# Kernel optimization log

Hardware: AMD Instinct MI355X
Metric: run time of the kernel (lower is better)

Reference implementation:

```python
import jax, jax.numpy as jnp
import numpy as np

IN_FEATURES = 4096
OUT_FEATURES = 4096
SHARED_ROWS = 256
BATCH = 8192


def setup_inputs() -> dict:
    key = jax.random.key(0)
    k_x, k_w, k_b = jax.random.split(key, 3)
    x = jax.random.normal(k_x, (BATCH, IN_FEATURES), dtype=jnp.float32)
    shared_weights = jax.random.normal(k_w, (SHARED_ROWS, IN_FEATURES), dtype=jnp.float32)
    bias = jax.random.normal(k_b, (OUT_FEATURES,), dtype=jnp.float32)
    return {"x": x, "shared_weights": shared_weights, "bias": bias}


def reference(x, shared_weights, bias):
    # Faithful to torch: weight_matrix = shared_weights.repeat(out//shared, 1)
    reps = OUT_FEATURES // SHARED_ROWS
    weight_matrix = jnp.tile(shared_weights, (reps, 1))  # [out_features, in_features]
    # y = x @ W^T + b  -> [batch, out_features]
    return jnp.matmul(x, weight_matrix.T) + bias
```

## Files before the change

kernel.cpp:

```cpp
#include <hip/hip_runtime.h>
#include <cstdint>
#include <cstddef>

#define M_DIM 8192
#define N_DIM 256
#define K_DIM 4096
#define OUT_F 4096
#define BM 32
#define BK 64
#define NTH 512
#define LDK 72

typedef float    float4_  __attribute__((ext_vector_type(4)));
typedef _Float16 half8    __attribute__((ext_vector_type(8)));
typedef _Float16 half4    __attribute__((ext_vector_type(4)));

__global__ __launch_bounds__(256) void convert_w_kernel(const float* __restrict__ w,
                                                        _Float16* __restrict__ wh) {
  int i = (blockIdx.x * 256 + threadIdx.x) * 8;
  float4_ f0 = *(const float4_*)(w + i);
  float4_ f1 = *(const float4_*)(w + i + 4);
  half8 h;
  h[0] = (_Float16)f0[0]; h[1] = (_Float16)f0[1];
  h[2] = (_Float16)f0[2]; h[3] = (_Float16)f0[3];
  h[4] = (_Float16)f1[0]; h[5] = (_Float16)f1[1];
  h[6] = (_Float16)f1[2]; h[7] = (_Float16)f1[3];
  *(half8*)(wh + i) = h;
}

__device__ __forceinline__ void load_bfrag(half8 b[2][2],
                                           const _Float16* __restrict__ wg0,
                                           const _Float16* __restrict__ wg1,
                                           int kk) {
#pragma unroll
  for (int ks = 0; ks < 2; ++ks) {
    b[ks][0] = *(const half8*)(wg0 + kk + ks * 32);
    b[ks][1] = *(const half8*)(wg1 + kk + ks * 32);
  }
}

__device__ __forceinline__ void stage_a(_Float16 (*As)[LDK], int arow, int acol,
                                        float4_ a) {
  half4 h;
  h[0] = (_Float16)a[0]; h[1] = (_Float16)a[1];
  h[2] = (_Float16)a[2]; h[3] = (_Float16)a[3];
  *(half4*)(&As[arow][acol]) = h;
}

__device__ __forceinline__ void mfma_step(float4_ acc[2][2], const half8 b[2][2],
                                          const _Float16 (*As)[LDK],
                                          int l16, int quad) {
#pragma unroll
  for (int ks = 0; ks < 2; ++ks) {
    const int koff = ks * 32 + quad * 8;
    half8 a0 = *(const half8*)(&As[l16][koff]);
    half8 a1 = *(const half8*)(&As[16 + l16][koff]);
    acc[0][0] = __builtin_amdgcn_mfma_f32_16x16x32_f16(a0, b[ks][0], acc[0][0], 0, 0, 0);
    acc[1][0] = __builtin_amdgcn_mfma_f32_16x16x32_f16(a1, b[ks][0], acc[1][0], 0, 0, 0);
    acc[0][1] = __builtin_amdgcn_mfma_f32_16x16x32_f16(a0, b[ks][1], acc[0][1], 0, 0, 0);
    acc[1][1] = __builtin_amdgcn_mfma_f32_16x16x32_f16(a1, b[ks][1], acc[1][1], 0, 0, 0);
  }
}

__global__ __launch_bounds__(NTH, 2) void fused_kernel(const float* __restrict__ x,
                                                       const _Float16* __restrict__ wh,
                                                       const float* __restrict__ bias,
                                                       float* __restrict__ out) {
  __shared__ __align__(16) _Float16 As[2][BM][LDK];
  __shared__ __align__(16) float Ssh[BM][N_DIM + 4];
  __shared__ __align__(16) float bsh[OUT_F];

  const int tid  = threadIdx.x;
  const int wv   = tid >> 6;
  const int lane = tid & 63;
  const int quad = lane >> 4;
  const int l16  = lane & 15;
  const int n0   = wv * 32;
  const int m0   = blockIdx.x * BM;

  {
    const float4_* b4 = (const float4_*)bias;
    float4_* bs4 = (float4_*)bsh;
    bs4[tid] = b4[tid];
    bs4[NTH + tid] = b4[NTH + tid];
  }

  const int arow = tid >> 4;
  const int acol = (tid & 15) * 4;
  const float* xg = x + (size_t)(m0 + arow) * K_DIM + acol;

  const _Float16* wg0 = wh + (size_t)(n0 + l16) * K_DIM + quad * 8;
  const _Float16* wg1 = wg0 + (size_t)16 * K_DIM;

  float4_ acc[2][2];
  const float4_ fzero = {0.f, 0.f, 0.f, 0.f};
#pragma unroll
  for (int i = 0; i < 2; ++i)
#pragma unroll
    for (int j = 0; j < 2; ++j) acc[i][j] = fzero;

  half8 bA[2][2], bB[2][2];
  float4_ aP0 = __builtin_nontemporal_load((const float4_*)(xg));
  float4_ aP1 = __builtin_nontemporal_load((const float4_*)(xg + BK));
  load_bfrag(bA, wg0, wg1, 0);
  stage_a(As[0], arow, acol, aP0);
  aP0 = __builtin_nontemporal_load((const float4_*)(xg + 2 * BK));
  __syncthreads();

  const int NKT = K_DIM / BK;
  for (int kt = 0; kt < NKT; kt += 2) {
    load_bfrag(bB, wg0, wg1, (kt + 1) * BK);
    stage_a(As[1], arow, acol, aP1);
    if (kt + 3 < NKT)
      aP1 = __builtin_nontemporal_load((const float4_*)(xg + (kt + 3) * BK));
    mfma_step(acc, bA, As[0], l16, quad);
    __syncthreads();

    if (kt + 2 < NKT) {
      load_bfrag(bA, wg0, wg1, (kt + 2) * BK);
      stage_a(As[0], arow, acol, aP0);
      if (kt + 4 < NKT)
        aP0 = __builtin_nontemporal_load((const float4_*)(xg + (kt + 4) * BK));
    }
    mfma_step(acc, bB, As[1], l16, quad);
    __syncthreads();
  }

#pragma unroll
  for (int mf = 0; mf < 2; ++mf)
#pragma unroll
    for (int nf = 0; nf < 2; ++nf)
#pragma unroll
      for (int r = 0; r < 4; ++r)
        Ssh[mf * 16 + quad * 4 + r][n0 + nf * 16 + l16] = acc[mf][nf][r];
  __syncthreads();

  float4_ s[4];
#pragma unroll
  for (int rr = 0; rr < 4; ++rr)
    s[rr] = *(const float4_*)(&Ssh[wv * 4 + rr][lane * 4]);

  float4_* o0 = (float4_*)(out + (size_t)(m0 + wv * 4) * OUT_F);
  const float4_* bs4 = (const float4_*)bsh;
#pragma unroll
  for (int i = 0; i < 16; ++i) {
    float4_ b4 = bs4[i * 64 + lane];
#pragma unroll
    for (int rr = 0; rr < 4; ++rr)
      __builtin_nontemporal_store(s[rr] + b4,
                                  o0 + (size_t)rr * (OUT_F / 4) + i * 64 + lane);
  }
}

extern "C" void kernel_launch(void* const* d_in, const int* in_sizes, int n_in,
                              void* d_out, int out_size, void* d_ws, size_t ws_size,
                              hipStream_t stream) {
  const float* x    = (const float*)d_in[0];
  const float* w    = (const float*)d_in[1];
  const float* bias = (const float*)d_in[2];
  float* out        = (float*)d_out;
  _Float16* wh      = (_Float16*)d_ws;

  convert_w_kernel<<<(N_DIM * K_DIM) / (256 * 8), 256, 0, stream>>>(w, wh);
  fused_kernel<<<M_DIM / BM, NTH, 0, stream>>>(x, wh, bias, out);
}
```

Before: 278.2 us.

## Split N across two blocks, swizzle A tile in LDS, raise occupancy

Splits the 256 shared output columns into two 128-wide halves via a second grid dimension, so each block does half the MMA work and twice as many blocks run. The padded A tile in LDS is replaced by an XOR-swizzled layout to avoid bank conflicts, and launch bounds ask for 4 blocks per CU. Nontemporal loads of x become normal loads so the two blocks sharing an x row-tile can hit in cache. The cost is that x is read twice (from cache or HBM) and fp32-to-fp16 conversion of A is duplicated.

```diff
diff --git a/kernel.cpp b/kernel.cpp
--- a/kernel.cpp
+++ b/kernel.cpp
@@ -7,9 +7,9 @@
 #define K_DIM 4096
 #define OUT_F 4096
 #define BM 32
+#define BN 128
 #define BK 64
 #define NTH 512
-#define LDK 72
 
 typedef float    float4_  __attribute__((ext_vector_type(4)));
 typedef _Float16 half8    __attribute__((ext_vector_type(8)));
@@ -28,99 +28,86 @@
   *(half8*)(wh + i) = h;
 }
 
-__device__ __forceinline__ void load_bfrag(half8 b[2][2],
-                                           const _Float16* __restrict__ wg0,
-                                           const _Float16* __restrict__ wg1,
+__device__ __forceinline__ void load_bfrag(half8 b[2], const _Float16* __restrict__ wg,
                                            int kk) {
-#pragma unroll
-  for (int ks = 0; ks < 2; ++ks) {
-    b[ks][0] = *(const half8*)(wg0 + kk + ks * 32);
-    b[ks][1] = *(const half8*)(wg1 + kk + ks * 32);
-  }
+  b[0] = *(const half8*)(wg + kk);
+  b[1] = *(const half8*)(wg + kk + 32);
 }
 
-__device__ __forceinline__ void stage_a(_Float16 (*As)[LDK], int arow, int acol,
+__device__ __forceinline__ void stage_a(_Float16* __restrict__ As, int arow, int asw,
                                         float4_ a) {
   half4 h;
   h[0] = (_Float16)a[0]; h[1] = (_Float16)a[1];
   h[2] = (_Float16)a[2]; h[3] = (_Float16)a[3];
-  *(half4*)(&As[arow][acol]) = h;
+  *(half4*)(As + arow * BK + asw) = h;
 }
 
-__device__ __forceinline__ void mfma_step(float4_ acc[2][2], const half8 b[2][2],
-                                          const _Float16 (*As)[LDK],
+__device__ __forceinline__ void mfma_step(float4_ acc[2], const half8 b[2],
+                                          const _Float16* __restrict__ As,
                                           int l16, int quad) {
 #pragma unroll
   for (int ks = 0; ks < 2; ++ks) {
-    const int koff = ks * 32 + quad * 8;
-    half8 a0 = *(const half8*)(&As[l16][koff]);
-    half8 a1 = *(const half8*)(&As[16 + l16][koff]);
-    acc[0][0] = __builtin_amdgcn_mfma_f32_16x16x32_f16(a0, b[ks][0], acc[0][0], 0, 0, 0);
-    acc[1][0] = __builtin_amdgcn_mfma_f32_16x16x32_f16(a1, b[ks][0], acc[1][0], 0, 0, 0);
-    acc[0][1] = __builtin_amdgcn_mfma_f32_16x16x32_f16(a0, b[ks][1], acc[0][1], 0, 0, 0);
-    acc[1][1] = __builtin_amdgcn_mfma_f32_16x16x32_f16(a1, b[ks][1], acc[1][1], 0, 0, 0);
+    const int off = ((ks * 4 + quad) ^ (l16 & 7)) << 3;
+    half8 a0 = *(const half8*)(As + l16 * BK + off);
+    half8 a1 = *(const half8*)(As + (16 + l16) * BK + off);
+    acc[0] = __builtin_amdgcn_mfma_f32_16x16x32_f16(a0, b[ks], acc[0], 0, 0, 0);
+    acc[1] = __builtin_amdgcn_mfma_f32_16x16x32_f16(a1, b[ks], acc[1], 0, 0, 0);
   }
 }
 
-__global__ __launch_bounds__(NTH, 2) void fused_kernel(const float* __restrict__ x,
+__global__ __launch_bounds__(NTH, 4) void fused_kernel(const float* __restrict__ x,
                                                        const _Float16* __restrict__ wh,
                                                        const float* __restrict__ bias,
                                                        float* __restrict__ out) {
-  __shared__ __align__(16) _Float16 As[2][BM][LDK];
-  __shared__ __align__(16) float Ssh[BM][N_DIM + 4];
-  __shared__ __align__(16) float bsh[OUT_F];
+  __shared__ __align__(16) _Float16 As[2][BM * BK];
+  __shared__ __align__(16) float Ssh[BM][BN + 4];
+  __shared__ __align__(16) float bsh[16 * BN];
 
   const int tid  = threadIdx.x;
   const int wv   = tid >> 6;
   const int lane = tid & 63;
   const int quad = lane >> 4;
   const int l16  = lane & 15;
-  const int n0   = wv * 32;
   const int m0   = blockIdx.x * BM;
+  const int nb   = blockIdx.y * BN;
 
   {
     const float4_* b4 = (const float4_*)bias;
     float4_* bs4 = (float4_*)bsh;
-    bs4[tid] = b4[tid];
-    bs4[NTH + tid] = b4[NTH + tid];
+    bs4[tid] = b4[(tid >> 5) * (N_DIM / 4) + (nb >> 2) + (tid & 31)];
   }
 
   const int arow = tid >> 4;
-  const int acol = (tid & 15) * 4;
-  const float* xg = x + (size_t)(m0 + arow) * K_DIM + acol;
+  const int ac4  = tid & 15;
+  const int asw  = ((((ac4 >> 1) ^ (arow & 7)) << 3) | ((ac4 & 1) << 2));
+  const float* xg = x + (size_t)(m0 + arow) * K_DIM + ac4 * 4;
 
-  const _Float16* wg0 = wh + (size_t)(n0 + l16) * K_DIM + quad * 8;
-  const _Float16* wg1 = wg0 + (size_t)16 * K_DIM;
+  const _Float16* wg = wh + (size_t)(nb + wv * 16 + l16) * K_DIM + quad * 8;
 
-  float4_ acc[2][2];
-  const float4_ fzero = {0.f, 0.f, 0.f, 0.f};
-#pragma unroll
-  for (int i = 0; i < 2; ++i)
-#pragma unroll
-    for (int j = 0; j < 2; ++j) acc[i][j] = fzero;
+  float4_ acc[2];
+  acc[0] = (float4_){0.f, 0.f, 0.f, 0.f};
+  acc[1] = (float4_){0.f, 0.f, 0.f, 0.f};
 
-  half8 bA[2][2], bB[2][2];
-  float4_ aP0 = __builtin_nontemporal_load((const float4_*)(xg));
-  float4_ aP1 = __builtin_nontemporal_load((const float4_*)(xg + BK));
-  load_bfrag(bA, wg0, wg1, 0);
-  stage_a(As[0], arow, acol, aP0);
-  aP0 = __builtin_nontemporal_load((const float4_*)(xg + 2 * BK));
+  half8 bA[2], bB[2];
+  float4_ aP0 = *(const float4_*)(xg);
+  float4_ aP1 = *(const float4_*)(xg + BK);
+  load_bfrag(bA, wg, 0);
+  stage_a(As[0], arow, asw, aP0);
+  aP0 = *(const float4_*)(xg + 2 * BK);
   __syncthreads();
 
   const int NKT = K_DIM / BK;
   for (int kt = 0; kt < NKT; kt += 2) {
-    load_bfrag(bB, wg0, wg1, (kt + 1) * BK);
-    stage_a(As[1], arow, acol, aP1);
-    if (kt + 3 < NKT)
-      aP1 = __builtin_nontemporal_load((const float4_*)(xg + (kt + 3) * BK));
+    load_bfrag(bB, wg, (kt + 1) * BK);
+    stage_a(As[1], arow, asw, aP1);
+    if (kt + 3 < NKT) aP1 = *(const float4_*)(xg + (kt + 3) * BK);
     mfma_step(acc, bA, As[0], l16, quad);
     __syncthreads();
 
     if (kt + 2 < NKT) {
-      load_bfrag(bA, wg0, wg1, (kt + 2) * BK);
-      stage_a(As[0], arow, acol, aP0);
-      if (kt + 4 < NKT)
-        aP0 = __builtin_nontemporal_load((const float4_*)(xg + (kt + 4) * BK));
+      load_bfrag(bA, wg, (kt + 2) * BK);
+      stage_a(As[0], arow, asw, aP0);
+      if (kt + 4 < NKT) aP0 = *(const float4_*)(xg + (kt + 4) * BK);
     }
     mfma_step(acc, bB, As[1], l16, quad);
     __syncthreads();
@@ -129,26 +116,22 @@
 #pragma unroll
   for (int mf = 0; mf < 2; ++mf)
 #pragma unroll
-    for (int nf = 0; nf < 2; ++nf)
-#pragma unroll
-      for (int r = 0; r < 4; ++r)
-        Ssh[mf * 16 + quad * 4 + r][n0 + nf * 16 + l16] = acc[mf][nf][r];
+    for (int r = 0; r < 4; ++r)
+      Ssh[mf * 16 + quad * 4 + r][wv * 16 + l16] = acc[mf][r];
   __syncthreads();
 
-  float4_ s[4];
-#pragma unroll
-  for (int rr = 0; rr < 4; ++rr)
-    s[rr] = *(const float4_*)(&Ssh[wv * 4 + rr][lane * 4]);
-
-  float4_* o0 = (float4_*)(out + (size_t)(m0 + wv * 4) * OUT_F);
+  float4_* out4 = (float4_*)out;
   const float4_* bs4 = (const float4_*)bsh;
 #pragma unroll
-  for (int i = 0; i < 16; ++i) {
-    float4_ b4 = bs4[i * 64 + lane];
+  for (int p = 0; p < 2; ++p) {
+    const int row = wv * 4 + p * 2 + (lane >> 5);
+    const int c4  = lane & 31;
+    float4_ sv = *(const float4_*)(&Ssh[row][c4 * 4]);
+    const size_t obase = (size_t)(m0 + row) * (OUT_F / 4) + (nb >> 2);
 #pragma unroll
-    for (int rr = 0; rr < 4; ++rr)
-      __builtin_nontemporal_store(s[rr] + b4,
-                                  o0 + (size_t)rr * (OUT_F / 4) + i * 64 + lane);
+    for (int rep = 0; rep < 16; ++rep)
+      __builtin_nontemporal_store(sv + bs4[rep * (BN / 4) + c4],
+                                  out4 + obase + rep * (N_DIM / 4) + c4);
   }
 }
 
@@ -162,5 +145,5 @@
   _Float16* wh      = (_Float16*)d_ws;
 
   convert_w_kernel<<<(N_DIM * K_DIM) / (256 * 8), 256, 0, stream>>>(w, wh);
-  fused_kernel<<<M_DIM / BM, NTH, 0, stream>>>(x, wh, bias, out);
+  fused_kernel<<<dim3(M_DIM / BM, 2), NTH, 0, stream>>>(x, wh, bias, out);
 }
```

New measurement: 270.6 us. 2.7% less time.
